# Kernel tuning notes

Measured on AMD Instinct MI355X. Metric: run time of the kernel, lower is better.

Reference implementation:

```python
import jax, jax.numpy as jnp
import numpy as np

B, T, F = 64, 512, 256
ENC = 256      # encoder output dim
P = 128        # projection_dim
H = 256        # gru_hidden_dim
K = 12         # num_future_steps
TEMP = 0.1


def setup_inputs() -> dict:
    key = jax.random.key(0)
    ks = jax.random.split(key, 12)
    s = lambda *d: 1.0 / np.sqrt(d[0])
    return {
        "x_seq": jax.random.normal(ks[0], (B, T, F), jnp.float32),
        # encoder: Dense(F -> ENC)
        "W_enc": jax.random.normal(ks[1], (F, ENC), jnp.float32) * s(F),
        "b_enc": jnp.zeros((ENC,), jnp.float32),
        # projection: Dense(ENC -> P)
        "W_proj": jax.random.normal(ks[2], (ENC, P), jnp.float32) * s(ENC),
        "b_proj": jnp.zeros((P,), jnp.float32),
        # GRUCell (flax convention: input dense has bias, hidden dense bias only on n)
        "Wi": jax.random.normal(ks[3], (P, 3 * H), jnp.float32) * s(P),
        "bi": jnp.zeros((3 * H,), jnp.float32),
        "Wh": jax.random.normal(ks[4], (H, 3 * H), jnp.float32) * s(H),
        "bhn": jnp.zeros((H,), jnp.float32),
        # K predictors: Dense(H -> P)
        "Wp": jax.random.normal(ks[5], (K, H, P), jnp.float32) * s(H),
        "bp": jnp.zeros((K, P), jnp.float32),
    }


def _gru_scan(z_seq, Wi, bi, Wh, bhn):
    # z_seq: [B, T, P] -> c_seq: [B, T, H]
    def step(h, x_t):
        gi = x_t @ Wi + bi          # [B, 3H]
        gh = h @ Wh                 # [B, 3H]
        ir, iz, inn = jnp.split(gi, 3, axis=-1)
        hr, hz, hn = jnp.split(gh, 3, axis=-1)
        r = jax.nn.sigmoid(ir + hr)
        z = jax.nn.sigmoid(iz + hz)
        n = jnp.tanh(inn + r * (hn + bhn))
        h_new = (1.0 - z) * n + z * h
        return h_new, h_new

    h0 = jnp.zeros((z_seq.shape[0], Wh.shape[0]), z_seq.dtype)
    _, c = jax.lax.scan(step, h0, jnp.swapaxes(z_seq, 0, 1))  # c: [T, B, H]
    return jnp.swapaxes(c, 0, 1)


def reference(x_seq, W_enc, b_enc, W_proj, b_proj, Wi, bi, Wh, bhn, Wp, bp):
    # encoder per timestep (vmap(vmap(Dense)) == batched matmul)
    z_seq = x_seq @ W_enc + b_enc                 # [B, T, ENC]
    z_seq = z_seq @ W_proj + b_proj               # [B, T, P]
    c_seq = _gru_scan(z_seq, Wi, bi, Wh, bhn)     # [B, T, H]

    Tlen = z_seq.shape[1]
    loss = jnp.asarray(0.0, z_seq.dtype)
    for k in range(1, K + 1):
        if Tlen - k <= 0:
            continue
        z_pos = z_seq[:, k:]                      # [B, T-k, P]
        pred = c_seq[:, :-k] @ Wp[k - 1] + bp[k - 1]  # [B, T-k, P]
        logits = jnp.einsum('btd,bkd->btk', pred, z_pos) / TEMP
        labels = jnp.arange(logits.shape[1])
        # NOTE: faithful to source: [..., labels] with labels=arange is an
        # identity gather along the last axis (not a diagonal pick).
        loss = loss + jnp.mean(-jax.nn.log_softmax(logits, axis=-1)[..., labels])
    return loss / K
```

## Files before the change

kernel.cpp:

```cpp
#include <hip/hip_runtime.h>
#include <hip/hip_bf16.h>
#include <math.h>

#define B_   64
#define T_   512
#define F_   256
#define ENC_ 256
#define P_   128
#define H_   256
#define K_   12
#define INV_TEMP 10.0f

typedef unsigned short u16;
typedef _Float16 half2v __attribute__((ext_vector_type(2)));
union U2H { unsigned int u; half2v h; };
typedef __attribute__((ext_vector_type(8))) short bf16x8;
typedef __attribute__((ext_vector_type(4))) float f32x4;
union BF8 { bf16x8 v; u16 e[8]; };

__device__ __forceinline__ float dot2f16(unsigned int a, unsigned int b, float c) {
    U2H ua; ua.u = a; U2H ub; ub.u = b;
#if __has_builtin(__builtin_amdgcn_fdot2)
    return __builtin_amdgcn_fdot2(ua.h, ub.h, c, false);
#else
    return fmaf((float)ua.h.x, (float)ub.h.x, fmaf((float)ua.h.y, (float)ub.h.y, c));
#endif
}
__device__ __forceinline__ float rcpf(float x) {
#if __has_builtin(__builtin_amdgcn_rcpf)
    return __builtin_amdgcn_rcpf(x);
#else
    return 1.f / x;
#endif
}
__device__ __forceinline__ u16 f2bf(float f) {
    unsigned int u = __float_as_uint(f);
    unsigned int r = (u + 0x7fffu + ((u >> 16) & 1u)) >> 16;
    return (u16)r;
}
__device__ __forceinline__ float bf2f(u16 v) {
    return __uint_as_float(((unsigned int)v) << 16);
}
__device__ __forceinline__ float bflo(unsigned int u) { return __uint_as_float(u << 16); }
__device__ __forceinline__ float bfhi(unsigned int u) { return __uint_as_float(u & 0xffff0000u); }
__device__ __forceinline__ float wave_sum(float v) {
    #pragma unroll
    for (int o = 32; o > 0; o >>= 1) v += __shfl_down(v, o, 64);
    return v;
}

__global__ __launch_bounds__(256) void setup_conv(const float* __restrict__ Wh,
                                                  uint2* __restrict__ Whh,
                                                  const float* __restrict__ Wi,
                                                  u16* __restrict__ Wit,
                                                  const float* __restrict__ Wp,
                                                  u16* __restrict__ Wpt,
                                                  const float* __restrict__ We,
                                                  const float* __restrict__ be,
                                                  const float* __restrict__ Wpj,
                                                  const float* __restrict__ bpj,
                                                  u16* __restrict__ Wct,
                                                  float* __restrict__ bc,
                                                  float* __restrict__ accum) {
    int bid = blockIdx.x;
    if (bid < 192) {
        int idx = bid * 256 + threadIdx.x;
        int i4 = idx / 768, j = idx % 768;
        U2H lo, hi;
        lo.h.x = (_Float16)Wh[(size_t)(4 * i4 + 0) * 768 + j];
        lo.h.y = (_Float16)Wh[(size_t)(4 * i4 + 1) * 768 + j];
        hi.h.x = (_Float16)Wh[(size_t)(4 * i4 + 2) * 768 + j];
        hi.h.y = (_Float16)Wh[(size_t)(4 * i4 + 3) * 768 + j];
        Whh[idx] = make_uint2(lo.u, hi.u);
    } else if (bid < 288) {
        __shared__ float tile[32][33];
        int b2 = bid - 192;
        int n0 = (b2 % 24) * 32, k0 = (b2 / 24) * 32;
        int tx = threadIdx.x & 31, ty = threadIdx.x >> 5;
        #pragma unroll
        for (int i = 0; i < 32; i += 8)
            tile[ty + i][tx] = Wi[(size_t)(k0 + ty + i) * 768 + n0 + tx];
        __syncthreads();
        #pragma unroll
        for (int i = 0; i < 32; i += 8)
            Wit[(size_t)(n0 + ty + i) * 128 + k0 + tx] = f2bf(tile[tx][ty + i]);
    } else if (bid < 672) {
        __shared__ float tile2[32][33];
        int b3 = bid - 288;
        int kq = b3 / 32, rem = b3 % 32;
        int h0 = (rem % 8) * 32, p0 = (rem / 8) * 32;
        int tx = threadIdx.x & 31, ty = threadIdx.x >> 5;
        #pragma unroll
        for (int i = 0; i < 32; i += 8)
            tile2[ty + i][tx] = Wp[(size_t)kq * H_ * P_ + (size_t)(h0 + ty + i) * P_ + p0 + tx];
        __syncthreads();
        #pragma unroll
        for (int i = 0; i < 32; i += 8)
            Wpt[(size_t)kq * P_ * H_ + (size_t)(p0 + ty + i) * H_ + h0 + tx] = f2bf(tile2[tx][ty + i]);
    } else {
        int f = (bid - 672) * 2 + (threadIdx.x >> 7);
        int p = threadIdx.x & 127;
        if (f < F_) {
            float a = 0.f;
            for (int e = 0; e < ENC_; e++) a = fmaf(We[f * ENC_ + e], Wpj[e * P_ + p], a);
            Wct[(size_t)p * F_ + f] = f2bf(a);
        } else if (f == F_) {
            float a = bpj[p];
            for (int e = 0; e < ENC_; e++) a = fmaf(be[e], Wpj[e * P_ + p], a);
            bc[p] = a;
        } else {
            #pragma unroll
            for (int i = 0; i < 8; i++) accum[p * 8 + i] = 0.f;
        }
    }
}

__global__ __launch_bounds__(256) void gemm_mfma_f32a(const float* __restrict__ A,
                                                      const u16* __restrict__ Bt,
                                                      const float* __restrict__ bias,
                                                      u16* __restrict__ Ch,
                                                      int N, int K) {
    int tid  = threadIdx.x;
    int w    = tid >> 6;
    int lane = tid & 63;
    int col  = lane & 15;
    int quad = lane >> 4;
    int bm = blockIdx.y * 64, bn = blockIdx.x * 128;

    f32x4 acc[8] = {};
    const float* arow = A + (size_t)(bm + w * 16 + col) * K;
    #pragma unroll
    for (int k0 = 0; k0 < K; k0 += 32) {
        float4 v0 = *(const float4*)(arow + k0 + quad * 8);
        float4 v1 = *(const float4*)(arow + k0 + quad * 8 + 4);
        BF8 af;
        af.e[0] = f2bf(v0.x); af.e[1] = f2bf(v0.y); af.e[2] = f2bf(v0.z); af.e[3] = f2bf(v0.w);
        af.e[4] = f2bf(v1.x); af.e[5] = f2bf(v1.y); af.e[6] = f2bf(v1.z); af.e[7] = f2bf(v1.w);
        #pragma unroll
        for (int nt = 0; nt < 8; nt++) {
            bf16x8 bf = *(const bf16x8*)(Bt + (size_t)(bn + nt * 16 + col) * K + k0 + quad * 8);
            acc[nt] = __builtin_amdgcn_mfma_f32_16x16x32_bf16(af.v, bf, acc[nt], 0, 0, 0);
        }
    }
    #pragma unroll
    for (int nt = 0; nt < 8; nt++) {
        int gn = bn + nt * 16 + col;
        float bv = bias[gn];
        #pragma unroll
        for (int r = 0; r < 4; r++) {
            int gm = bm + w * 16 + quad * 4 + r;
            Ch[(size_t)gm * N + gn] = f2bf(acc[nt][r] + bv);
        }
    }
}

__global__ __launch_bounds__(256) void gemm_mfma(const u16* __restrict__ A,
                                                 const u16* __restrict__ Bt,
                                                 const float* __restrict__ bias,
                                                 u16* __restrict__ Ch,
                                                 int N, int K) {
    int tid  = threadIdx.x;
    int w    = tid >> 6;
    int lane = tid & 63;
    int col  = lane & 15;
    int quad = lane >> 4;
    int bm = blockIdx.y * 64, bn = blockIdx.x * 128;

    f32x4 acc[8] = {};
    const u16* arow = A + (size_t)(bm + w * 16 + col) * K;
    #pragma unroll
    for (int k0 = 0; k0 < K; k0 += 32) {
        bf16x8 af = *(const bf16x8*)(arow + k0 + quad * 8);
        #pragma unroll
        for (int nt = 0; nt < 8; nt++) {
            bf16x8 bf = *(const bf16x8*)(Bt + (size_t)(bn + nt * 16 + col) * K + k0 + quad * 8);
            acc[nt] = __builtin_amdgcn_mfma_f32_16x16x32_bf16(af, bf, acc[nt], 0, 0, 0);
        }
    }
    #pragma unroll
    for (int nt = 0; nt < 8; nt++) {
        int gn = bn + nt * 16 + col;
        float bv = bias[gn];
        #pragma unroll
        for (int r = 0; r < 4; r++) {
            int gm = bm + w * 16 + quad * 4 + r;
            Ch[(size_t)gm * N + gn] = f2bf(acc[nt][r] + bv);
        }
    }
}

__global__ __attribute__((amdgpu_flat_work_group_size(512, 512), amdgpu_waves_per_eu(2, 2)))
void gru_zsum_kernel(const u16* __restrict__ gi,
                     const uint2* __restrict__ Whh,
                     const float* __restrict__ bhn,
                     u16* __restrict__ ch,
                     const u16* __restrict__ zh,
                     float* __restrict__ zsum) {
    __shared__ __align__(16) char shraw[8704];
    int tid = threadIdx.x;

    if (blockIdx.x >= B_) {
        float (*part)[128] = (float(*)[128])shraw;
        int b   = blockIdx.x - B_;
        int pg  = tid & 31;
        int g   = tid >> 5;
        const u16* zb = zh + (size_t)b * T_ * P_;
        float s0 = 0.f, s1 = 0.f, s2 = 0.f, s3 = 0.f;
        for (int t = 1 + g; t < T_; t += 16) {
            uint2 v = *(const uint2*)(zb + (size_t)t * P_ + pg * 4);
            s0 += bflo(v.x); s1 += bfhi(v.x);
            s2 += bflo(v.y); s3 += bfhi(v.y);
        }
        part[g][pg * 4 + 0] = s0; part[g][pg * 4 + 1] = s1;
        part[g][pg * 4 + 2] = s2; part[g][pg * 4 + 3] = s3;
        __syncthreads();
        if (tid < 128) {
            float s = 0.f;
            #pragma unroll
            for (int g2 = 0; g2 < 16; g2++) s += part[g2][tid];
            zsum[(size_t)b * P_ + tid] = s;
        }
        return;
    }

    _Float16* hbuf = (_Float16*)shraw;
    float4 (*ps)[256] = (float4(*)[256])(shraw + 512);
    int b    = blockIdx.x;
    int j    = tid & 255;
    int half = tid >> 8;

    uint2 wR[32], wZ[32], wN[32];
    {
        const uint2* base = Whh + (size_t)(half * 32) * 768;
        const uint2* cR = base + j;
        const uint2* cZ = base + 256 + j;
        const uint2* cN = base + 512 + j;
        #pragma unroll
        for (int i = 0; i < 32; i++) {
            wR[i] = cR[(size_t)i * 768];
            wZ[i] = cZ[(size_t)i * 768];
            wN[i] = cN[(size_t)i * 768];
        }
        #pragma unroll
        for (int i = 0; i < 32; i++) {
            asm volatile("" : "+v"(wR[i].x), "+v"(wR[i].y));
            asm volatile("" : "+v"(wZ[i].x), "+v"(wZ[i].y));
            asm volatile("" : "+v"(wN[i].x), "+v"(wN[i].y));
        }
    }
    if (tid < H_) hbuf[tid] = (_Float16)0.f;
    float bh = bhn[j];
    float hloc = 0.f;

    const u16* gib = gi + (size_t)b * T_ * 768;
    u16* cb = ch + (size_t)b * T_ * H_;
    float ir = 0.f, iz = 0.f, inn = 0.f;
    if (tid < 256) { ir = bf2f(gib[j]); iz = bf2f(gib[256 + j]); inn = bf2f(gib[512 + j]); }
    __syncthreads();

    const uint2* hw = (const uint2*)hbuf;
    #pragma unroll 1
    for (int t = 0; t < T_; t++) {
        float nir = 0.f, niz = 0.f, ninn = 0.f;
        if (tid < 256) {
            int tn = (t + 1 < T_) ? t + 1 : t;
            const u16* gtn = gib + (size_t)tn * 768;
            nir = bf2f(gtn[j]); niz = bf2f(gtn[256 + j]); ninn = bf2f(gtn[512 + j]);
        }
        float ar0 = 0.f, ar1 = 0.f, az0 = 0.f, az1 = 0.f, an0 = 0.f, an1 = 0.f;
        #pragma unroll
        for (int i = 0; i < 32; i++) {
            uint2 hv = hw[half * 32 + i];
            ar0 = dot2f16(hv.x, wR[i].x, ar0);
            ar1 = dot2f16(hv.y, wR[i].y, ar1);
            az0 = dot2f16(hv.x, wZ[i].x, az0);
            az1 = dot2f16(hv.y, wZ[i].y, az1);
            an0 = dot2f16(hv.x, wN[i].x, an0);
            an1 = dot2f16(hv.y, wN[i].y, an1);
        }
        ps[half][j] = make_float4(ar0 + ar1, az0 + az1, an0 + an1, 0.f);
        __syncthreads();
        if (tid < 256) {
            float4 p0 = ps[0][j], p1 = ps[1][j];
            float ar = p0.x + p1.x;
            float az = p0.y + p1.y;
            float an = p0.z + p1.z;
            float r   = rcpf(1.f + __expf(-(ir + ar)));
            float zg  = rcpf(1.f + __expf(-(iz + az)));
            float xn  = inn + r * (an + bh);
            float n   = fmaf(2.f, rcpf(1.f + __expf(-2.f * xn)), -1.f);
            hloc = (1.f - zg) * n + zg * hloc;
            cb[(size_t)t * H_ + j] = f2bf(hloc);
            hbuf[j] = (_Float16)hloc;
        }
        ir = nir; iz = niz; inn = ninn;
        __syncthreads();
    }
}

__global__ __launch_bounds__(512) void loss_fused(const u16* __restrict__ ch,
                                                  const u16* __restrict__ Wpt,
                                                  const float* __restrict__ bp,
                                                  const u16* __restrict__ zh,
                                                  const float* __restrict__ zsum,
                                                  float* __restrict__ accum) {
    __shared__ u16 Pst[128][136];
    __shared__ u16 Zt[64][136];
    __shared__ float sS[128];
    __shared__ float red[8];
    int k  = blockIdx.z + 1;
    int b  = blockIdx.y;
    int t0 = blockIdx.x * 128;
    int Tk = T_ - k;
    int tid  = threadIdx.x;
    int w    = tid >> 6;
    int lane = tid & 63;
    int col  = lane & 15;
    int quad = lane >> 4;
    const u16* zb = zh + (size_t)b * T_ * P_;

    if (tid < 128) {
        float s = zsum[(size_t)b * P_ + tid];
        for (int t = 1; t < k; t++) s -= bf2f(zb[(size_t)t * P_ + tid]);
        sS[tid] = s;
    }

    {
        f32x4 acc[8] = {};
        const u16* arow = ch + ((size_t)b * T_ + t0 + w * 16 + col) * H_;
        const u16* wk   = Wpt + (size_t)(k - 1) * P_ * H_;
        #pragma unroll
        for (int k0 = 0; k0 < 8; k0++) {
            bf16x8 af = *(const bf16x8*)(arow + k0 * 32 + quad * 8);
            #pragma unroll
            for (int nt = 0; nt < 8; nt++) {
                bf16x8 bf = *(const bf16x8*)(wk + (size_t)(nt * 16 + col) * H_ + k0 * 32 + quad * 8);
                acc[nt] = __builtin_amdgcn_mfma_f32_16x16x32_bf16(af, bf, acc[nt], 0, 0, 0);
            }
        }
        #pragma unroll
        for (int nt = 0; nt < 8; nt++) {
            float bias = bp[(size_t)(k - 1) * P_ + nt * 16 + col];
            #pragma unroll
            for (int r = 0; r < 4; r++)
                Pst[w * 16 + quad * 4 + r][nt * 16 + col] = f2bf(acc[nt][r] + bias);
        }
    }
    __syncthreads();

    float mloc[4], sloc[4];
    #pragma unroll
    for (int r = 0; r < 4; r++) { mloc[r] = -INFINITY; sloc[r] = 0.f; }

    for (int ct = 0; ct < Tk; ct += 64) {
        __syncthreads();
        {
            int cc = tid;
            #pragma unroll
            for (int rep = 0; rep < 2; rep++, cc += 512) {
                int row = cc >> 4;
                int off = (cc & 15) * 8;
                int tcol = k + ct + row;
                *(uint4*)&Zt[row][off] = *(const uint4*)(zb + (size_t)tcol * P_ + off);
            }
        }
        __syncthreads();
        f32x4 acc[4] = {};
        #pragma unroll
        for (int k0 = 0; k0 < 4; k0++) {
            bf16x8 af = *(const bf16x8*)(&Pst[w * 16 + col][k0 * 32 + quad * 8]);
            #pragma unroll
            for (int nt = 0; nt < 4; nt++) {
                bf16x8 bf = *(const bf16x8*)(&Zt[nt * 16 + col][k0 * 32 + quad * 8]);
                acc[nt] = __builtin_amdgcn_mfma_f32_16x16x32_bf16(af, bf, acc[nt], 0, 0, 0);
            }
        }
        #pragma unroll
        for (int r = 0; r < 4; r++) {
            float l[4];
            float tmax = -INFINITY;
            #pragma unroll
            for (int nt = 0; nt < 4; nt++) {
                bool valid = (ct + nt * 16 + col) < Tk;
                l[nt] = valid ? acc[nt][r] * INV_TEMP : -INFINITY;
                tmax = fmaxf(tmax, l[nt]);
            }
            float mnew = fmaxf(mloc[r], tmax);
            float e = __expf(l[0] - mnew) + __expf(l[1] - mnew)
                    + __expf(l[2] - mnew) + __expf(l[3] - mnew);
            sloc[r] = sloc[r] * __expf(mloc[r] - mnew) + e;
            mloc[r] = mnew;
        }
    }
    #pragma unroll
    for (int r = 0; r < 4; r++) {
        #pragma unroll
        for (int o = 1; o < 16; o <<= 1) {
            float mo = __shfl_xor(mloc[r], o, 64);
            float so = __shfl_xor(sloc[r], o, 64);
            float mn = fmaxf(mloc[r], mo);
            sloc[r] = sloc[r] * __expf(mloc[r] - mn) + so * __expf(mo - mn);
            mloc[r] = mn;
        }
    }
    float tkinv = INV_TEMP / (float)Tk;
    float scale = 1.0f / ((float)K_ * (float)B_ * (float)Tk);
    float bs = 0.f;
    #pragma unroll
    for (int r = 0; r < 4; r++) {
        int row = w * 16 + quad * 4 + r;
        BF8 pv;
        pv.v = *(const bf16x8*)(&Pst[row][col * 8]);
        float d = 0.f;
        #pragma unroll
        for (int m = 0; m < 8; m++) d = fmaf(bf2f(pv.e[m]), sS[col * 8 + m], d);
        #pragma unroll
        for (int o = 1; o < 16; o <<= 1) d += __shfl_xor(d, o, 64);
        int gr = t0 + row;
        if (gr < Tk) bs += mloc[r] + __logf(sloc[r]) - d * tkinv;
    }
    if (col != 0) bs = 0.f;
    bs = wave_sum(bs);
    if (lane == 0) red[w] = bs;
    __syncthreads();
    if (tid == 0) {
        float tot = 0.f;
        #pragma unroll
        for (int i = 0; i < 8; i++) tot += red[i];
        atomicAdd(&accum[(blockIdx.x * 809 + b * 67 + blockIdx.z * 131) & 1023],
                  tot * scale);
    }
}

__global__ void finalize(const float* __restrict__ accum, float* __restrict__ out) {
    int tid = threadIdx.x;
    __shared__ float red[4];
    float v = 0.f;
    for (int i = tid; i < 1024; i += 256) v += accum[i];
    float sres = wave_sum(v);
    if ((tid & 63) == 0) red[tid >> 6] = sres;
    __syncthreads();
    if (tid == 0) out[0] = red[0] + red[1] + red[2] + red[3];
}

extern "C" void kernel_launch(void* const* d_in, const int* in_sizes, int n_in,
                              void* d_out, int out_size, void* d_ws, size_t ws_size,
                              hipStream_t stream) {
    const float* x      = (const float*)d_in[0];
    const float* W_enc  = (const float*)d_in[1];
    const float* b_enc  = (const float*)d_in[2];
    const float* W_proj = (const float*)d_in[3];
    const float* b_proj = (const float*)d_in[4];
    const float* Wi     = (const float*)d_in[5];
    const float* bi     = (const float*)d_in[6];
    const float* Wh     = (const float*)d_in[7];
    const float* bhn    = (const float*)d_in[8];
    const float* Wp     = (const float*)d_in[9];
    const float* bp     = (const float*)d_in[10];
    float* out = (float*)d_out;

    float* ws    = (float*)d_ws;
    float* bc    = ws;
    float* accum = bc + 128;
    uint2* Whh   = (uint2*)(ws + 1152);
    u16* Wct     = (u16*)(ws + 99456);
    u16* Wit     = (u16*)(ws + 115840);
    u16* Wpt     = (u16*)(ws + 164992);
    u16* zh      = (u16*)(ws + 361600);
    float* zsum  = ws + 2458752;
    u16* gi      = (u16*)(ws + 2466944);
    u16* ch      = (u16*)(ws + 15049856);

    const int MT = B_ * T_;

    setup_conv<<<801, 256, 0, stream>>>(Wh, Whh, Wi, Wit, Wp, Wpt,
                                        W_enc, b_enc, W_proj, b_proj, Wct, bc, accum);
    gemm_mfma_f32a<<<dim3(1, MT / 64), 256, 0, stream>>>(x, Wct, bc, zh, P_, F_);
    gemm_mfma<<<dim3(6, MT / 64), 256, 0, stream>>>(zh, Wit, bi, gi, 3 * H_, P_);
    gru_zsum_kernel<<<2 * B_, 512, 0, stream>>>(gi, Whh, bhn, ch, zh, zsum);
    loss_fused<<<dim3(4, B_, K_), 512, 0, stream>>>(ch, Wpt, bp, zh, zsum, accum);
    finalize<<<1, 256, 0, stream>>>(accum, out);
}
```

Baseline: 1.057 ms.

## Batch GRU recurrence across 16 sequences per block using fp16 MFMA

Replaces the per-sequence GRU (one block per batch row, dot2 over register-resident weights) with 4 blocks, each handling 16 batch rows. The h@Wh product becomes a 16-row MFMA with the weights held as f16 fragments in registers. The input gates are prefetched into a double-buffered LDS area via async global-to-LDS loads, and the hidden state is double-buffered so each step needs only one barrier. Setup now writes Wh transposed in fp16 to match. This cuts the sequential per-step cost and the weight traffic, but only 4 CUs run the recurrence, so per-step latency across MFMA chains and LDS decides the outcome.

```diff
diff --git a/kernel.cpp b/kernel.cpp
--- a/kernel.cpp
+++ b/kernel.cpp
@@ -16,16 +16,9 @@
 union U2H { unsigned int u; half2v h; };
 typedef __attribute__((ext_vector_type(8))) short bf16x8;
 typedef __attribute__((ext_vector_type(4))) float f32x4;
+typedef _Float16 f16x8 __attribute__((ext_vector_type(8)));
 union BF8 { bf16x8 v; u16 e[8]; };
 
-__device__ __forceinline__ float dot2f16(unsigned int a, unsigned int b, float c) {
-    U2H ua; ua.u = a; U2H ub; ub.u = b;
-#if __has_builtin(__builtin_amdgcn_fdot2)
-    return __builtin_amdgcn_fdot2(ua.h, ub.h, c, false);
-#else
-    return fmaf((float)ua.h.x, (float)ub.h.x, fmaf((float)ua.h.y, (float)ub.h.y, c));
-#endif
-}
 __device__ __forceinline__ float rcpf(float x) {
 #if __has_builtin(__builtin_amdgcn_rcpf)
     return __builtin_amdgcn_rcpf(x);
@@ -50,7 +43,7 @@
 }
 
 __global__ __launch_bounds__(256) void setup_conv(const float* __restrict__ Wh,
-                                                  uint2* __restrict__ Whh,
+                                                  _Float16* __restrict__ Wht,
                                                   const float* __restrict__ Wi,
                                                   u16* __restrict__ Wit,
                                                   const float* __restrict__ Wp,
@@ -64,14 +57,16 @@
                                                   float* __restrict__ accum) {
     int bid = blockIdx.x;
     if (bid < 192) {
-        int idx = bid * 256 + threadIdx.x;
-        int i4 = idx / 768, j = idx % 768;
-        U2H lo, hi;
-        lo.h.x = (_Float16)Wh[(size_t)(4 * i4 + 0) * 768 + j];
-        lo.h.y = (_Float16)Wh[(size_t)(4 * i4 + 1) * 768 + j];
-        hi.h.x = (_Float16)Wh[(size_t)(4 * i4 + 2) * 768 + j];
-        hi.h.y = (_Float16)Wh[(size_t)(4 * i4 + 3) * 768 + j];
-        Whh[idx] = make_uint2(lo.u, hi.u);
+        __shared__ float tile0[32][33];
+        int g0 = (bid % 24) * 32, k0 = (bid / 24) * 32;
+        int tx = threadIdx.x & 31, ty = threadIdx.x >> 5;
+        #pragma unroll
+        for (int i = 0; i < 32; i += 8)
+            tile0[ty + i][tx] = Wh[(size_t)(k0 + ty + i) * 768 + g0 + tx];
+        __syncthreads();
+        #pragma unroll
+        for (int i = 0; i < 32; i += 8)
+            Wht[(size_t)(g0 + ty + i) * 256 + k0 + tx] = (_Float16)tile0[tx][ty + i];
     } else if (bid < 288) {
         __shared__ float tile[32][33];
         int b2 = bid - 192;
@@ -189,19 +184,22 @@
     }
 }
 
+#define GRUB_ 4
+#define BPB_  16
+
 __global__ __attribute__((amdgpu_flat_work_group_size(512, 512), amdgpu_waves_per_eu(2, 2)))
 void gru_zsum_kernel(const u16* __restrict__ gi,
-                     const uint2* __restrict__ Whh,
+                     const _Float16* __restrict__ Wht,
                      const float* __restrict__ bhn,
                      u16* __restrict__ ch,
                      const u16* __restrict__ zh,
                      float* __restrict__ zsum) {
-    __shared__ __align__(16) char shraw[8704];
+    __shared__ __align__(16) char smem[66048];
     int tid = threadIdx.x;
 
-    if (blockIdx.x >= B_) {
-        float (*part)[128] = (float(*)[128])shraw;
-        int b   = blockIdx.x - B_;
+    if (blockIdx.x >= GRUB_) {
+        float (*part)[128] = (float (*)[128])smem;
+        int b   = blockIdx.x - GRUB_;
         int pg  = tid & 31;
         int g   = tid >> 5;
         const u16* zb = zh + (size_t)b * T_ * P_;
@@ -223,78 +221,103 @@
         return;
     }
 
-    _Float16* hbuf = (_Float16*)shraw;
-    float4 (*ps)[256] = (float4(*)[256])(shraw + 512);
-    int b    = blockIdx.x;
-    int j    = tid & 255;
-    int half = tid >> 8;
-
-    uint2 wR[32], wZ[32], wN[32];
-    {
-        const uint2* base = Whh + (size_t)(half * 32) * 768;
-        const uint2* cR = base + j;
-        const uint2* cZ = base + 256 + j;
-        const uint2* cN = base + 512 + j;
-        #pragma unroll
-        for (int i = 0; i < 32; i++) {
-            wR[i] = cR[(size_t)i * 768];
-            wZ[i] = cZ[(size_t)i * 768];
-            wN[i] = cN[(size_t)i * 768];
-        }
-        #pragma unroll
-        for (int i = 0; i < 32; i++) {
-            asm volatile("" : "+v"(wR[i].x), "+v"(wR[i].y));
-            asm volatile("" : "+v"(wZ[i].x), "+v"(wZ[i].y));
-            asm volatile("" : "+v"(wN[i].x), "+v"(wN[i].y));
-        }
-    }
-    if (tid < H_) hbuf[tid] = (_Float16)0.f;
-    float bh = bhn[j];
-    float hloc = 0.f;
-
-    const u16* gib = gi + (size_t)b * T_ * 768;
-    u16* cb = ch + (size_t)b * T_ * H_;
-    float ir = 0.f, iz = 0.f, inn = 0.f;
-    if (tid < 256) { ir = bf2f(gib[j]); iz = bf2f(gib[256 + j]); inn = bf2f(gib[512 + j]); }
+    _Float16 (*hb)[16][264] = (_Float16 (*)[16][264])smem;
+    u16 (*gils)[16][768]    = (u16 (*)[16][768])(smem + 16896);
+
+    int lane = tid & 63, w = tid >> 6;
+    int col  = lane & 15, quad = lane >> 4;
+    int bb   = blockIdx.x * BPB_;
+    int jj0  = w * 32 + col;
+
+    f16x8 wf[3][2][8];
+    #pragma unroll
+    for (int g = 0; g < 3; g++)
+        #pragma unroll
+        for (int n2 = 0; n2 < 2; n2++) {
+            const _Float16* src = Wht + (size_t)(g * 256 + jj0 + n2 * 16) * 256 + quad * 8;
+            #pragma unroll
+            for (int k0 = 0; k0 < 8; k0++)
+                wf[g][n2][k0] = *(const f16x8*)(src + k0 * 32);
+        }
+    #pragma unroll
+    for (int g = 0; g < 3; g++)
+        #pragma unroll
+        for (int n2 = 0; n2 < 2; n2++)
+            #pragma unroll
+            for (int k0 = 0; k0 < 8; k0++)
+                asm volatile("" : "+v"(wf[g][n2][k0]));
+
+    for (int i = tid; i < 2 * 16 * 264; i += 512) ((_Float16*)hb)[i] = (_Float16)0.f;
+
+    const u16* gp[3];
+    #pragma unroll
+    for (int rr = 0; rr < 3; rr++) {
+        int off = (rr * 512 + tid) * 8;
+        int bt = off / 768, bo = off - bt * 768;
+        gp[rr] = gi + (size_t)(bb + bt) * T_ * 768 + bo;
+    }
+    #pragma unroll
+    for (int rr = 0; rr < 3; rr++) {
+        __builtin_amdgcn_global_load_lds(
+            (const __attribute__((address_space(1))) void*)gp[rr],
+            (__attribute__((address_space(3))) void*)(&gils[0][0][0] + (rr * 512 + w * 64) * 8),
+            16, 0, 0);
+        gp[rr] += 768;
+    }
+
+    float bh0 = bhn[jj0], bh1 = bhn[jj0 + 16];
+    float hold[2][4] = {};
+    u16* chp0 = ch + (size_t)(bb + quad * 4) * T_ * 256 + jj0;
+
     __syncthreads();
 
-    const uint2* hw = (const uint2*)hbuf;
+    int cur = 0;
     #pragma unroll 1
     for (int t = 0; t < T_; t++) {
-        float nir = 0.f, niz = 0.f, ninn = 0.f;
-        if (tid < 256) {
-            int tn = (t + 1 < T_) ? t + 1 : t;
-            const u16* gtn = gib + (size_t)tn * 768;
-            nir = bf2f(gtn[j]); niz = bf2f(gtn[256 + j]); ninn = bf2f(gtn[512 + j]);
-        }
-        float ar0 = 0.f, ar1 = 0.f, az0 = 0.f, az1 = 0.f, an0 = 0.f, an1 = 0.f;
-        #pragma unroll
-        for (int i = 0; i < 32; i++) {
-            uint2 hv = hw[half * 32 + i];
-            ar0 = dot2f16(hv.x, wR[i].x, ar0);
-            ar1 = dot2f16(hv.y, wR[i].y, ar1);
-            az0 = dot2f16(hv.x, wZ[i].x, az0);
-            az1 = dot2f16(hv.y, wZ[i].y, az1);
-            an0 = dot2f16(hv.x, wN[i].x, an0);
-            an1 = dot2f16(hv.y, wN[i].y, an1);
-        }
-        ps[half][j] = make_float4(ar0 + ar1, az0 + az1, an0 + an1, 0.f);
-        __syncthreads();
-        if (tid < 256) {
-            float4 p0 = ps[0][j], p1 = ps[1][j];
-            float ar = p0.x + p1.x;
-            float az = p0.y + p1.y;
-            float an = p0.z + p1.z;
-            float r   = rcpf(1.f + __expf(-(ir + ar)));
-            float zg  = rcpf(1.f + __expf(-(iz + az)));
-            float xn  = inn + r * (an + bh);
-            float n   = fmaf(2.f, rcpf(1.f + __expf(-2.f * xn)), -1.f);
-            hloc = (1.f - zg) * n + zg * hloc;
-            cb[(size_t)t * H_ + j] = f2bf(hloc);
-            hbuf[j] = (_Float16)hloc;
-        }
-        ir = nir; iz = niz; inn = ninn;
-        __syncthreads();
+        int nxt = cur ^ 1;
+        if (t + 1 < T_) {
+            #pragma unroll
+            for (int rr = 0; rr < 3; rr++) {
+                __builtin_amdgcn_global_load_lds(
+                    (const __attribute__((address_space(1))) void*)gp[rr],
+                    (__attribute__((address_space(3))) void*)(&gils[nxt][0][0] + (rr * 512 + w * 64) * 8),
+                    16, 0, 0);
+                gp[rr] += 768;
+            }
+        }
+        f32x4 acc[3][2] = {};
+        #pragma unroll
+        for (int k0 = 0; k0 < 8; k0++) {
+            f16x8 af = *(const f16x8*)(&hb[cur][col][k0 * 32 + quad * 8]);
+            #pragma unroll
+            for (int g = 0; g < 3; g++)
+                #pragma unroll
+                for (int n2 = 0; n2 < 2; n2++)
+                    acc[g][n2] = __builtin_amdgcn_mfma_f32_16x16x32_f16(af, wf[g][n2][k0], acc[g][n2], 0, 0, 0);
+        }
+        int tof = t * 256;
+        #pragma unroll
+        for (int n2 = 0; n2 < 2; n2++) {
+            int jj = jj0 + n2 * 16;
+            float bh = n2 ? bh1 : bh0;
+            #pragma unroll
+            for (int r = 0; r < 4; r++) {
+                int b = quad * 4 + r;
+                float ir  = bf2f(gils[cur][b][jj]);
+                float iz  = bf2f(gils[cur][b][256 + jj]);
+                float inn = bf2f(gils[cur][b][512 + jj]);
+                float rg  = rcpf(1.f + __expf(-(ir + acc[0][n2][r])));
+                float zg  = rcpf(1.f + __expf(-(iz + acc[1][n2][r])));
+                float xn  = inn + rg * (acc[2][n2][r] + bh);
+                float nn  = fmaf(2.f, rcpf(1.f + __expf(-2.f * xn)), -1.f);
+                float hv  = (1.f - zg) * nn + zg * hold[n2][r];
+                hold[n2][r] = hv;
+                hb[nxt][b][jj] = (_Float16)hv;
+                chp0[r * (T_ * 256) + tof + n2 * 16] = f2bf(hv);
+            }
+        }
+        __syncthreads();
+        cur = nxt;
     }
 }
 
@@ -462,7 +485,7 @@
     float* ws    = (float*)d_ws;
     float* bc    = ws;
     float* accum = bc + 128;
-    uint2* Whh   = (uint2*)(ws + 1152);
+    _Float16* Wht = (_Float16*)(ws + 1152);
     u16* Wct     = (u16*)(ws + 99456);
     u16* Wit     = (u16*)(ws + 115840);
     u16* Wpt     = (u16*)(ws + 164992);
@@ -473,11 +496,11 @@
 
     const int MT = B_ * T_;
 
-    setup_conv<<<801, 256, 0, stream>>>(Wh, Whh, Wi, Wit, Wp, Wpt,
+    setup_conv<<<801, 256, 0, stream>>>(Wh, Wht, Wi, Wit, Wp, Wpt,
                                         W_enc, b_enc, W_proj, b_proj, Wct, bc, accum);
     gemm_mfma_f32a<<<dim3(1, MT / 64), 256, 0, stream>>>(x, Wct, bc, zh, P_, F_);
     gemm_mfma<<<dim3(6, MT / 64), 256, 0, stream>>>(zh, Wit, bi, gi, 3 * H_, P_);
-    gru_zsum_kernel<<<2 * B_, 512, 0, stream>>>(gi, Whh, bhn, ch, zh, zsum);
+    gru_zsum_kernel<<<GRUB_ + B_, 512, 0, stream>>>(gi, Wht, bhn, ch, zh, zsum);
     loss_fused<<<dim3(4, B_, K_), 512, 0, stream>>>(ch, Wpt, bp, zh, zsum, accum);
     finalize<<<1, 256, 0, stream>>>(accum, out);
 }
```

Measured after the change: 1.500 ms. 42.0% more time.
